# Optimization experiments

Hardware: AMD Instinct MI355X
Metric: run time of the kernel (lower is better)

The kernel has to match this reference:

```python
import jax, jax.numpy as jnp
import numpy as np

N = 30000   # nodes
E = 480000  # edges (avg degree 16)
D = 256     # feat_dim == dim
H = 8       # heads
C = 32      # out channels per head (D // H, concat=True)
NEG = 0.2   # leaky-relu negative slope (args.alpha)
L = 2       # num_layers
NENC = 2 * L  # two GATv2 encoders (source/target direction) per layer


def setup_inputs() -> dict:
    key = jax.random.key(0)
    ks = jax.random.split(key, 10)
    s = jax.random.normal(ks[0], (N, D), dtype=jnp.float32)
    t = jax.random.normal(ks[1], (N, D), dtype=jnp.float32)
    edge_index = jax.random.randint(ks[2], (2, E), 0, N, dtype=jnp.int32)
    scale = 0.05
    Wl = jax.random.normal(ks[3], (NENC, D, H * C), dtype=jnp.float32) * scale
    bl = jnp.zeros((NENC, H * C), dtype=jnp.float32)
    Wr = jax.random.normal(ks[4], (NENC, D, H * C), dtype=jnp.float32) * scale
    br = jnp.zeros((NENC, H * C), dtype=jnp.float32)
    att = jax.random.normal(ks[5], (NENC, H, C), dtype=jnp.float32) * scale
    bias = jnp.zeros((NENC, H * C), dtype=jnp.float32)
    return {"s": s, "t": t, "Wl": Wl, "bl": bl, "Wr": Wr, "br": br,
            "att": att, "bias": bias, "edge_index": edge_index}


def _gatv2(x_src, x_dst, src, dst, Wl, bl, Wr, br, att, bias):
    """PyG GATv2Conv on bipartite input ((x_src, x_dst), edge_index).
    Messages flow src->dst, softmax-normalized over incoming edges of dst."""
    hl = (x_src @ Wl + bl).reshape(N, H, C)  # lin_l(source)
    hr = (x_dst @ Wr + br).reshape(N, H, C)  # lin_r(target)
    xe = hl[src] + hr[dst]                    # [E,H,C]
    e = jnp.where(xe > 0, xe, NEG * xe)       # leaky_relu
    logits = jnp.einsum('ehc,hc->eh', e, att)  # [E,H]
    m = jax.ops.segment_max(logits, dst, num_segments=N)
    m = jnp.where(jnp.isfinite(m), m, jnp.zeros_like(m))  # empty segments
    p = jnp.exp(logits - m[dst])
    denom = jax.ops.segment_sum(p, dst, num_segments=N)
    alpha = p / (denom[dst] + 1e-16)          # scatter-softmax weights [E,H]
    out = jax.ops.segment_sum(alpha[:, :, None] * hl[src], dst, num_segments=N)
    return out.reshape(N, H * C) + bias       # concat heads + bias


def reference(s, t, Wl, bl, Wr, br, att, bias, edge_index):
    src, dst = edge_index[0], edge_index[1]
    x_s, x_t = s, t
    for l in range(L):
        i, j = 2 * l, 2 * l + 1
        # source_encoder((s, t), edges): aggregate s-messages at t-nodes
        sh = _gatv2(x_s, x_t, src, dst, Wl[i], bl[i], Wr[i], br[i], att[i], bias[i])
        # target_encoder((t, s), flipped edges)
        th = _gatv2(x_t, x_s, dst, src, Wl[j], bl[j], Wr[j], br[j], att[j], bias[j])
        if l < L - 1:  # last layer activation is identity
            sh = jax.nn.relu(sh)
            th = jax.nn.relu(th)
        x_s, x_t = sh, th
    return x_s, x_t
```

## Files before the change

### kernel.cpp

```cpp
#include <hip/hip_runtime.h>
#include <hip/hip_bf16.h>

#define NNODES 30000
#define NEDGES 480000
#define HC 256
#define NEG_SLOPE 0.2f
#define NPART 8
#define EPP 60000
#define PN (NPART * NNODES)
#define SCAN_CHUNK 1024
#define NCHUNK2 235
#define NCHUNKM 30
#define CPP 235
#define NFE 7680000

typedef _Float16 half8 __attribute__((ext_vector_type(8)));
typedef _Float16 h4v __attribute__((ext_vector_type(4)));
typedef _Float16 h2 __attribute__((ext_vector_type(2)));
typedef float floatx4 __attribute__((ext_vector_type(4)));


__global__ void prep_kernel(const float* __restrict__ Wl, const float* __restrict__ Wr,
                            _Float16* __restrict__ WtL, _Float16* __restrict__ WtR,
                            const int* __restrict__ ei, int* __restrict__ deg_dst,
                            int* __restrict__ deg_src) {
    __shared__ float sh[32][33];
    int b = blockIdx.x;
    if (b < 512) {
        int e = b >> 6;
        int r0 = ((b >> 3) & 7) * 32, c0 = (b & 7) * 32;
        const float* W = (e < 4) ? Wl + (size_t)e * 65536 : Wr + (size_t)(e - 4) * 65536;
        _Float16* Wt = (e < 4) ? WtL + (size_t)e * 65536 : WtR + (size_t)(e - 4) * 65536;
        int x = threadIdx.x & 31, y = threadIdx.x >> 5;
#pragma unroll
        for (int j = 0; j < 4; j++) {
            int r = y + j * 8;
            sh[r][x] = W[(size_t)(r0 + r) * 256 + c0 + x];
        }
        __syncthreads();
#pragma unroll
        for (int j = 0; j < 4; j++) {
            int nn = y + j * 8;
            Wt[(size_t)(c0 + nn) * 256 + r0 + x] = (_Float16)sh[x][nn];
        }
    } else {
        b -= 512;
        int p = b & 7, c = b >> 3;
        int idx = c * 256 + threadIdx.x;
        if (idx >= EPP) return;
        int e = p * EPP + idx;
        int s = ei[e];
        int d = ei[NEDGES + e];
        atomicAdd(&deg_dst[p * NNODES + d], 1);
        atomicAdd(&deg_src[p * NNODES + s], 1);
    }
}

__global__ void mdeg_kernel(const int* __restrict__ deg_dst, const int* __restrict__ deg_src,
                            int* __restrict__ mdeg_dst, int* __restrict__ mdeg_src) {
    const int* deg = blockIdx.y ? deg_src : deg_dst;
    int* mdeg = blockIdx.y ? mdeg_src : mdeg_dst;
    int n = blockIdx.x * blockDim.x + threadIdx.x;
    if (n >= NNODES) return;
    int s = 0;
#pragma unroll
    for (int p = 0; p < NPART; p++) s += deg[p * NNODES + n];
    mdeg[n] = s;
}


__global__ void scanA_kernel(const int* __restrict__ deg_dst, const int* __restrict__ deg_src,
                             const int* __restrict__ mdeg_dst, const int* __restrict__ mdeg_src,
                             int* __restrict__ cur_dst, int* __restrict__ cur_src,
                             int* __restrict__ mrp_dst, int* __restrict__ mrp_src,
                             int* __restrict__ bsum) {
    __shared__ int sh[SCAN_CHUNK];
    const int y = blockIdx.y;
    const int nelem = (y < 2) ? PN : NNODES;
    if (blockIdx.x * SCAN_CHUNK >= nelem) return;
    const int* in = (y == 0) ? deg_dst : (y == 1) ? deg_src : (y == 2) ? mdeg_dst : mdeg_src;
    int t = threadIdx.x;
    int gid = blockIdx.x * SCAN_CHUNK + t;
    int v = (gid < nelem) ? in[gid] : 0;
    sh[t] = v;
    __syncthreads();
    for (int off = 1; off < SCAN_CHUNK; off <<= 1) {
        int u = (t >= off) ? sh[t - off] : 0;
        __syncthreads();
        sh[t] += u;
        __syncthreads();
    }
    if (gid < nelem) {
        if (y < 2) {
            int* cur = (y == 0) ? cur_dst : cur_src;
            cur[gid] = sh[t] - v;
        } else {
            int* mrp = (y == 2) ? mrp_dst : mrp_src;
            mrp[gid + 1] = sh[t];
        }
    }
    if (t == SCAN_CHUNK - 1) bsum[y * 256 + blockIdx.x] = sh[t];
}

__global__ void scan2_kernel(int* __restrict__ bsum) {
    int t = threadIdx.x;
    if (t < 4) {
        int cnt = (t < 2) ? NCHUNK2 : NCHUNKM;
        int run = 0;
        for (int i = 0; i < cnt; i++) {
            int v = bsum[t * 256 + i];
            bsum[t * 256 + i] = run;
            run += v;
        }
    }
}

__global__ void scanB_kernel(int* __restrict__ cur_dst, int* __restrict__ cur_src,
                             int* __restrict__ mrp_dst, int* __restrict__ mrp_src,
                             const int* __restrict__ bsum) {
    const int y = blockIdx.y;
    const int nelem = (y < 2) ? PN : NNODES;
    if (blockIdx.x * SCAN_CHUNK >= nelem) return;
    int t = threadIdx.x;
    int gid = blockIdx.x * SCAN_CHUNK + t;
    int base = bsum[y * 256 + blockIdx.x];
    if (gid < nelem) {
        if (y < 2) {
            ((y == 0) ? cur_dst : cur_src)[gid] += base;
        } else {
            ((y == 2) ? mrp_dst : mrp_src)[gid + 1] += base;
        }
    }
    if (gid == 0 && y >= 2) ((y == 2) ? mrp_dst : mrp_src)[0] = 0;
}

__global__ void fill_kernel(const int* __restrict__ ei, int* __restrict__ cur_dst,
                            int* __restrict__ cur_src, unsigned short* __restrict__ col_dst,
                            unsigned short* __restrict__ col_src) {
    int p = blockIdx.x & 7, c = blockIdx.x >> 3;
    int idx = c * 256 + threadIdx.x;
    if (idx >= EPP) return;
    int e = p * EPP + idx;
    int s = ei[e];
    int d = ei[NEDGES + e];
    int p0 = atomicAdd(&cur_dst[p * NNODES + d], 1);
    col_dst[p0] = (unsigned short)s;
    int p1 = atomicAdd(&cur_src[p * NNODES + s], 1);
    col_src[p1] = (unsigned short)d;
}

__global__ void merge_kernel(const int* __restrict__ deg_dst, const int* __restrict__ deg_src,
                             const int* __restrict__ cur_dst, const int* __restrict__ cur_src,
                             const int* __restrict__ mrp_dst, const int* __restrict__ mrp_src,
                             const unsigned short* __restrict__ col_dst,
                             const unsigned short* __restrict__ col_src,
                             unsigned short* __restrict__ mcol_dst,
                             unsigned short* __restrict__ mcol_src) {
    const int z = blockIdx.y;
    const int* deg = z ? deg_src : deg_dst;
    const int* cur = z ? cur_src : cur_dst;
    const int* mrp = z ? mrp_src : mrp_dst;
    const unsigned short* col = z ? col_src : col_dst;
    unsigned short* mcol = z ? mcol_src : mcol_dst;
    int n = blockIdx.x * blockDim.x + threadIdx.x;
    if (n >= NNODES) return;
    int w = mrp[n];
#pragma unroll
    for (int p = 0; p < NPART; p++) {
        int e = cur[p * NNODES + n];
        int d = deg[p * NNODES + n];
        for (int k = e - d; k < e; k++) mcol[w++] = col[k];
    }
}


__device__ inline half8 ldA8(const _Float16* p) { return *(const half8*)p; }
__device__ inline half8 ldA8(const float* p) {
    float4 a = *(const float4*)p;
    float4 b = *(const float4*)(p + 4);
    half8 r = {(_Float16)a.x, (_Float16)a.y, (_Float16)a.z, (_Float16)a.w,
               (_Float16)b.x, (_Float16)b.y, (_Float16)b.z, (_Float16)b.w};
    return r;
}

#define EPI_STRIDE 264

template <typename AT>
__global__ void __launch_bounds__(256)
gemm_f16(const AT* __restrict__ xs, const AT* __restrict__ xt,
         const _Float16* __restrict__ WtL, const _Float16* __restrict__ WtR,
         const float* __restrict__ bl, const float* __restrict__ br,
         _Float16* __restrict__ hbase, int e0) {
    const int y = blockIdx.y;
    const int e = e0 + (y >> 1);
    const AT* A = (y == 0 || y == 3) ? xs : xt;
    const bool left = (y & 1) == 0;
    const _Float16* Wt = (left ? WtL : WtR) + (size_t)e * 65536;
    const float* bvec = (left ? bl : br) + (size_t)e * HC;
    _Float16* C = hbase + (size_t)y * NFE;

    __shared__ __align__(16) _Float16 sh[10240];
    _Float16* As = sh;
    _Float16* Bs = sh + 2048;

    const int t = threadIdx.x;
    const int lane = t & 63, w = t >> 6;
    const int m0 = blockIdx.x * 64;
    const int rl = lane & 15, ch = lane >> 4;
    const int ar = t >> 2, ac = t & 3;

    floatx4 acc[4][4] = {};

    half8 av = {};
    {
        int gr = m0 + ar;
        if (gr < NNODES) av = ldA8(A + (size_t)gr * 256 + ac * 8);
    }
    half8 bv[4];
#pragma unroll
    for (int j = 0; j < 4; j++)
        bv[j] = *(const half8*)(Wt + (size_t)(ar + j * 64) * 256 + ac * 8);

    for (int k0 = 0; k0 < 256; k0 += 32) {
        __syncthreads();
        *(half8*)(As + ar * 32 + (ac ^ ((ar >> 1) & 3)) * 8) = av;
#pragma unroll
        for (int j = 0; j < 4; j++) {
            int n = ar + j * 64;
            *(half8*)(Bs + n * 32 + (ac ^ ((n >> 1) & 3)) * 8) = bv[j];
        }
        __syncthreads();

        if (k0 + 32 < 256) {
            int gr = m0 + ar;
            if (gr < NNODES) av = ldA8(A + (size_t)gr * 256 + (k0 + 32) + ac * 8);
#pragma unroll
            for (int j = 0; j < 4; j++)
                bv[j] = *(const half8*)(Wt + (size_t)(ar + j * 64) * 256 + (k0 + 32) + ac * 8);
        }

        half8 a[4], b[4];
#pragma unroll
        for (int fm = 0; fm < 4; fm++) {
            int r = fm * 16 + rl;
            a[fm] = *(const half8*)(As + r * 32 + (ch ^ ((r >> 1) & 3)) * 8);
        }
#pragma unroll
        for (int fn = 0; fn < 4; fn++) {
            int n = w * 64 + fn * 16 + rl;
            b[fn] = *(const half8*)(Bs + n * 32 + (ch ^ ((n >> 1) & 3)) * 8);
        }
#pragma unroll
        for (int fm = 0; fm < 4; fm++)
#pragma unroll
            for (int fn = 0; fn < 4; fn++)
                acc[fm][fn] = __builtin_amdgcn_mfma_f32_16x16x32_f16(a[fm], b[fn], acc[fm][fn], 0, 0, 0);
    }

    float bb[4];
#pragma unroll
    for (int fn = 0; fn < 4; fn++) bb[fn] = bvec[w * 64 + fn * 16 + rl];

#pragma unroll
    for (int hh = 0; hh < 2; hh++) {
        __syncthreads();
#pragma unroll
        for (int f2 = 0; f2 < 2; f2++) {
            int fm = hh * 2 + f2;
#pragma unroll
            for (int fn = 0; fn < 4; fn++) {
                int colb = w * 64 + fn * 16 + rl;
#pragma unroll
                for (int j = 0; j < 4; j++) {
                    int lr = f2 * 16 + ch * 4 + j;
                    sh[lr * EPI_STRIDE + colb] = (_Float16)(acc[fm][fn][j] + bb[fn]);
                }
            }
        }
        __syncthreads();
        int lr = t >> 3;
        int cseg = (t & 7) * 32;
        int gr = m0 + hh * 32 + lr;
        if (gr < NNODES) {
#pragma unroll
            for (int q = 0; q < 4; q++)
                *(half8*)(C + (size_t)gr * 256 + cseg + q * 8) =
                    *(const half8*)(sh + lr * EPI_STRIDE + cseg + q * 8);
        }
    }
}


__device__ __forceinline__ void edge_body(half8 hv, half8 hrv, const float* att8,
                                          float* acc, float& denom, bool valid) {
    const h2 negv = {(_Float16)NEG_SLOPE, (_Float16)NEG_SLOPE};
    const h2* hvp = (const h2*)&hv;
    const h2* hrp = (const h2*)&hrv;
    float v = 0.f;
#pragma unroll
    for (int k = 0; k < 4; k++) {
        h2 x = hvp[k] + hrp[k];
        h2 lk = __builtin_elementwise_max(x, x * negv);
        v = fmaf((float)lk[0], att8[2 * k], v);
        v = fmaf((float)lk[1], att8[2 * k + 1], v);
    }
    v += __shfl_xor(v, 1);
    v += __shfl_xor(v, 2);
    float pe = __expf(v);
    if (!valid) pe = 0.f;
    denom += pe;
#pragma unroll
    for (int k = 0; k < 8; k++) acc[k] = fmaf((float)hv[k], pe, acc[k]);
}

__device__ inline void store8(float* p, const float* o) {
    *(float4*)p = make_float4(o[0], o[1], o[2], o[3]);
    *(float4*)(p + 4) = make_float4(o[4], o[5], o[6], o[7]);
}
__device__ inline void store8(_Float16* p, const float* o) {
    half8 h = {(_Float16)o[0], (_Float16)o[1], (_Float16)o[2], (_Float16)o[3],
               (_Float16)o[4], (_Float16)o[5], (_Float16)o[6], (_Float16)o[7]};
    *(half8*)p = h;
}

template <typename OT>
__global__ void __launch_bounds__(256)
agg_kernel(const _Float16* __restrict__ hbase,
           const int* __restrict__ mrp_dst, const unsigned short* __restrict__ mcol_dst,
           const int* __restrict__ mrp_src, const unsigned short* __restrict__ mcol_src,
           const float* __restrict__ att, const float* __restrict__ bias,
           OT* __restrict__ out0, OT* __restrict__ out1, int e0, int do_relu) {
    const int z = blockIdx.y;
    const _Float16* hl = hbase + (size_t)z * 2 * NFE;
    const _Float16* hr = hl + NFE;
    const int* mrp = z ? mrp_src : mrp_dst;
    const unsigned short* mcol = z ? mcol_src : mcol_dst;
    const float* attz = att + (size_t)(e0 + z) * HC;
    const float* biasz = bias + (size_t)(e0 + z) * HC;
    OT* out = z ? out1 : out0;

    int wave = threadIdx.x >> 6;
    int lane = threadIdx.x & 63;
    int n = blockIdx.x * 4 + wave;
    if (n >= NNODES) return;
    int h = lane >> 5;
    int cl = lane & 31;
    int c8 = cl << 3;

    const _Float16* hlc = hl + c8;
    half8 hrv = *(const half8*)(hr + (size_t)n * HC + c8);
    float att8[8];
    *(float4*)(att8) = *(const float4*)(attz + c8);
    *(float4*)(att8 + 4) = *(const float4*)(attz + c8 + 4);

    float acc[8] = {};
    float denom = 0.f;
    int beg = mrp[n], end = mrp[n + 1];

    int i = beg;
    for (; i + 8 <= end; i += 8) {
        int s0 = (int)mcol[i + h];
        int s1 = (int)mcol[i + 2 + h];
        int s2 = (int)mcol[i + 4 + h];
        int s3 = (int)mcol[i + 6 + h];
        half8 hv0 = *(const half8*)(hlc + ((size_t)s0 << 8));
        half8 hv1 = *(const half8*)(hlc + ((size_t)s1 << 8));
        half8 hv2 = *(const half8*)(hlc + ((size_t)s2 << 8));
        half8 hv3 = *(const half8*)(hlc + ((size_t)s3 << 8));
        edge_body(hv0, hrv, att8, acc, denom, true);
        edge_body(hv1, hrv, att8, acc, denom, true);
        edge_body(hv2, hrv, att8, acc, denom, true);
        edge_body(hv3, hrv, att8, acc, denom, true);
    }
    for (; i + 2 <= end; i += 2) {
        int s0 = (int)mcol[i + h];
        half8 hv0 = *(const half8*)(hlc + ((size_t)s0 << 8));
        edge_body(hv0, hrv, att8, acc, denom, true);
    }
    if (i < end) {
        bool valid = (h == 0);
        int s0 = (int)mcol[i];
        half8 hv0 = *(const half8*)(hlc + ((size_t)s0 << 8));
        edge_body(hv0, hrv, att8, acc, denom, valid);
    }

#pragma unroll
    for (int k = 0; k < 8; k++) acc[k] += __shfl_xor(acc[k], 32);
    denom += __shfl_xor(denom, 32);

    if (lane < 32) {
        float inv = 1.f / (denom + 1e-16f);
        float o[8];
        float b8[8];
        *(float4*)(b8) = *(const float4*)(biasz + c8);
        *(float4*)(b8 + 4) = *(const float4*)(biasz + c8 + 4);
#pragma unroll
        for (int k = 0; k < 8; k++) {
            o[k] = acc[k] * inv + b8[k];
            if (do_relu) o[k] = fmaxf(o[k], 0.f);
        }
        store8(out + (size_t)n * HC + c8, o);
    }
}


extern "C" void kernel_launch(void* const* d_in, const int* in_sizes, int n_in,
                              void* d_out, int out_size, void* d_ws, size_t ws_size,
                              hipStream_t stream) {
    const float* s = (const float*)d_in[0];
    const float* t = (const float*)d_in[1];
    const float* Wl = (const float*)d_in[2];
    const float* bl = (const float*)d_in[3];
    const float* Wr = (const float*)d_in[4];
    const float* br = (const float*)d_in[5];
    const float* att = (const float*)d_in[6];
    const float* bias = (const float*)d_in[7];
    const int* ei = (const int*)d_in[8];
    float* out = (float*)d_out;

    const size_t NF = (size_t)NFE;

    _Float16* os16 = (_Float16*)d_ws;
    _Float16* ot16 = os16 + NF;
    _Float16* hbase = ot16 + NF;
    _Float16* WtL = hbase + 4 * NF;
    _Float16* WtR = WtL + 4 * 65536;
    int* deg_dst = (int*)(WtR + 4 * 65536);
    int* deg_src = deg_dst + PN;
    int* cur_dst = deg_src + PN;
    int* cur_src = cur_dst + PN;
    int* mdeg_dst = cur_src + PN;
    int* mdeg_src = mdeg_dst + NNODES;
    int* mrp_dst = mdeg_src + NNODES;
    int* mrp_src = mrp_dst + (NNODES + 1);
    int* bsum = mrp_src + (NNODES + 1);
    unsigned short* col_dst = (unsigned short*)(bsum + 1024);
    unsigned short* col_src = col_dst + NEDGES;
    unsigned short* mcol_dst = col_src + NEDGES;
    unsigned short* mcol_src = mcol_dst + NEDGES;

    hipMemsetAsync(deg_dst, 0, 2 * PN * sizeof(int), stream);
    prep_kernel<<<512 + NPART * CPP, 256, 0, stream>>>(Wl, Wr, WtL, WtR, ei, deg_dst, deg_src);
    mdeg_kernel<<<dim3(118, 2), 256, 0, stream>>>(deg_dst, deg_src, mdeg_dst, mdeg_src);
    {
        dim3 g(NCHUNK2, 4);
        scanA_kernel<<<g, SCAN_CHUNK, 0, stream>>>(deg_dst, deg_src, mdeg_dst, mdeg_src,
                                                   cur_dst, cur_src, mrp_dst, mrp_src, bsum);
        scan2_kernel<<<1, 64, 0, stream>>>(bsum);
        scanB_kernel<<<g, SCAN_CHUNK, 0, stream>>>(cur_dst, cur_src, mrp_dst, mrp_src, bsum);
    }
    fill_kernel<<<NPART * CPP, 256, 0, stream>>>(ei, cur_dst, cur_src, col_dst, col_src);
    merge_kernel<<<dim3(118, 2), 256, 0, stream>>>(deg_dst, deg_src, cur_dst, cur_src,
                                                   mrp_dst, mrp_src, col_dst, col_src,
                                                   mcol_dst, mcol_src);

    dim3 ggemm((NNODES + 63) / 64, 4);
    dim3 gagg((NNODES + 3) / 4, 2);

    gemm_f16<float><<<ggemm, 256, 0, stream>>>(s, t, WtL, WtR, bl, br, hbase, 0);
    agg_kernel<_Float16><<<gagg, 256, 0, stream>>>(hbase, mrp_dst, mcol_dst, mrp_src, mcol_src,
                                                   att, bias, os16, ot16, 0, 1);
    gemm_f16<_Float16><<<ggemm, 256, 0, stream>>>(os16, ot16, WtL, WtR, bl, br, hbase, 2);
    agg_kernel<float><<<gagg, 256, 0, stream>>>(hbase, mrp_dst, mcol_dst, mrp_src, mcol_src,
                                                att, bias, out, out + NF, 2, 0);
}
```

Measured before the change: 377.6 us.

## Split aggregation per head with 8-edge parallel waves and fuse degree merge into scan

The aggregation kernel now assigns one wave per (node, head) pair, with 8 lanes covering the head's 32 channels (4 each) and 8 edges processed in parallel per iteration. Attention logits use packed fp16 dot products, and partial sums are reduced across the edge groups at the end. The separate mdeg kernel is removed; the scan kernel sums the per-partition degrees directly. This aims to raise occupancy and parallelism per node and to cut one launch, at the cost of 8x more blocks and more shuffle reductions, plus fp16 dot precision for the logits.

Measured after the change: 648.8 us. 1.72x slower.

```diff
diff --git a/kernel.cpp b/kernel.cpp
--- a/kernel.cpp
+++ b/kernel.cpp
@@ -56,21 +56,8 @@
     }
 }
 
-__global__ void mdeg_kernel(const int* __restrict__ deg_dst, const int* __restrict__ deg_src,
-                            int* __restrict__ mdeg_dst, int* __restrict__ mdeg_src) {
-    const int* deg = blockIdx.y ? deg_src : deg_dst;
-    int* mdeg = blockIdx.y ? mdeg_src : mdeg_dst;
-    int n = blockIdx.x * blockDim.x + threadIdx.x;
-    if (n >= NNODES) return;
-    int s = 0;
-#pragma unroll
-    for (int p = 0; p < NPART; p++) s += deg[p * NNODES + n];
-    mdeg[n] = s;
-}
-
 
 __global__ void scanA_kernel(const int* __restrict__ deg_dst, const int* __restrict__ deg_src,
-                             const int* __restrict__ mdeg_dst, const int* __restrict__ mdeg_src,
                              int* __restrict__ cur_dst, int* __restrict__ cur_src,
                              int* __restrict__ mrp_dst, int* __restrict__ mrp_src,
                              int* __restrict__ bsum) {
@@ -78,10 +65,18 @@
     const int y = blockIdx.y;
     const int nelem = (y < 2) ? PN : NNODES;
     if (blockIdx.x * SCAN_CHUNK >= nelem) return;
-    const int* in = (y == 0) ? deg_dst : (y == 1) ? deg_src : (y == 2) ? mdeg_dst : mdeg_src;
     int t = threadIdx.x;
     int gid = blockIdx.x * SCAN_CHUNK + t;
-    int v = (gid < nelem) ? in[gid] : 0;
+    int v = 0;
+    if (gid < nelem) {
+        if (y == 0) v = deg_dst[gid];
+        else if (y == 1) v = deg_src[gid];
+        else {
+            const int* deg = (y == 2) ? deg_dst : deg_src;
+#pragma unroll
+            for (int p = 0; p < NPART; p++) v += deg[p * NNODES + gid];
+        }
+    }
     sh[t] = v;
     __syncthreads();
     for (int off = 1; off < SCAN_CHUNK; off <<= 1) {
@@ -92,11 +87,9 @@
     }
     if (gid < nelem) {
         if (y < 2) {
-            int* cur = (y == 0) ? cur_dst : cur_src;
-            cur[gid] = sh[t] - v;
+            ((y == 0) ? cur_dst : cur_src)[gid] = sh[t] - v;
         } else {
-            int* mrp = (y == 2) ? mrp_dst : mrp_src;
-            mrp[gid + 1] = sh[t];
+            ((y == 2) ? mrp_dst : mrp_src)[gid + 1] = sh[t];
         }
     }
     if (t == SCAN_CHUNK - 1) bsum[y * 256 + blockIdx.x] = sh[t];
@@ -291,36 +284,13 @@
 }
 
 
-__device__ __forceinline__ void edge_body(half8 hv, half8 hrv, const float* att8,
-                                          float* acc, float& denom, bool valid) {
-    const h2 negv = {(_Float16)NEG_SLOPE, (_Float16)NEG_SLOPE};
-    const h2* hvp = (const h2*)&hv;
-    const h2* hrp = (const h2*)&hrv;
-    float v = 0.f;
-#pragma unroll
-    for (int k = 0; k < 4; k++) {
-        h2 x = hvp[k] + hrp[k];
-        h2 lk = __builtin_elementwise_max(x, x * negv);
-        v = fmaf((float)lk[0], att8[2 * k], v);
-        v = fmaf((float)lk[1], att8[2 * k + 1], v);
-    }
-    v += __shfl_xor(v, 1);
-    v += __shfl_xor(v, 2);
-    float pe = __expf(v);
-    if (!valid) pe = 0.f;
-    denom += pe;
-#pragma unroll
-    for (int k = 0; k < 8; k++) acc[k] = fmaf((float)hv[k], pe, acc[k]);
-}
-
-__device__ inline void store8(float* p, const float* o) {
-    *(float4*)p = make_float4(o[0], o[1], o[2], o[3]);
-    *(float4*)(p + 4) = make_float4(o[4], o[5], o[6], o[7]);
-}
-__device__ inline void store8(_Float16* p, const float* o) {
-    half8 h = {(_Float16)o[0], (_Float16)o[1], (_Float16)o[2], (_Float16)o[3],
-               (_Float16)o[4], (_Float16)o[5], (_Float16)o[6], (_Float16)o[7]};
-    *(half8*)p = h;
+__device__ inline void stslice(float* p, float o0, float o1, float o2, float o3) {
+    floatx4 v = {o0, o1, o2, o3};
+    *(floatx4*)p = v;
+}
+__device__ inline void stslice(_Float16* p, float o0, float o1, float o2, float o3) {
+    h4v h = {(_Float16)o0, (_Float16)o1, (_Float16)o2, (_Float16)o3};
+    *(h4v*)p = h;
 }
 
 template <typename OT>
@@ -339,67 +309,73 @@
     const float* biasz = bias + (size_t)(e0 + z) * HC;
     OT* out = z ? out1 : out0;
 
-    int wave = threadIdx.x >> 6;
-    int lane = threadIdx.x & 63;
-    int n = blockIdx.x * 4 + wave;
+    const int wave = threadIdx.x >> 6;
+    const int lane = threadIdx.x & 63;
+    const int head = blockIdx.x & 7;
+    const int n = (blockIdx.x >> 3) * 4 + wave;
     if (n >= NNODES) return;
-    int h = lane >> 5;
-    int cl = lane & 31;
-    int c8 = cl << 3;
-
-    const _Float16* hlc = hl + c8;
-    half8 hrv = *(const half8*)(hr + (size_t)n * HC + c8);
-    float att8[8];
-    *(float4*)(att8) = *(const float4*)(attz + c8);
-    *(float4*)(att8 + 4) = *(const float4*)(attz + c8 + 4);
-
-    float acc[8] = {};
-    float denom = 0.f;
+    const int g = lane >> 3;
+    const int cl = lane & 7;
+    const int c = (head << 5) + (cl << 2);
+
+    const _Float16* hlc = hl + c;
+    h4v hrv = *(const h4v*)(hr + (size_t)n * HC + c);
+    float4 a4 = *(const float4*)(attz + c);
+    const h2 at0 = {(_Float16)a4.x, (_Float16)a4.y};
+    const h2 at1 = {(_Float16)a4.z, (_Float16)a4.w};
+    const h2 negv = {(_Float16)NEG_SLOPE, (_Float16)NEG_SLOPE};
+    const h2 hr0 = {hrv[0], hrv[1]};
+    const h2 hr1 = {hrv[2], hrv[3]};
+
+    float acc0 = 0.f, acc1 = 0.f, acc2 = 0.f, acc3 = 0.f, denom = 0.f;
     int beg = mrp[n], end = mrp[n + 1];
 
-    int i = beg;
-    for (; i + 8 <= end; i += 8) {
-        int s0 = (int)mcol[i + h];
-        int s1 = (int)mcol[i + 2 + h];
-        int s2 = (int)mcol[i + 4 + h];
-        int s3 = (int)mcol[i + 6 + h];
-        half8 hv0 = *(const half8*)(hlc + ((size_t)s0 << 8));
-        half8 hv1 = *(const half8*)(hlc + ((size_t)s1 << 8));
-        half8 hv2 = *(const half8*)(hlc + ((size_t)s2 << 8));
-        half8 hv3 = *(const half8*)(hlc + ((size_t)s3 << 8));
-        edge_body(hv0, hrv, att8, acc, denom, true);
-        edge_body(hv1, hrv, att8, acc, denom, true);
-        edge_body(hv2, hrv, att8, acc, denom, true);
-        edge_body(hv3, hrv, att8, acc, denom, true);
-    }
-    for (; i + 2 <= end; i += 2) {
-        int s0 = (int)mcol[i + h];
-        half8 hv0 = *(const half8*)(hlc + ((size_t)s0 << 8));
-        edge_body(hv0, hrv, att8, acc, denom, true);
-    }
-    if (i < end) {
-        bool valid = (h == 0);
-        int s0 = (int)mcol[i];
-        half8 hv0 = *(const half8*)(hlc + ((size_t)s0 << 8));
-        edge_body(hv0, hrv, att8, acc, denom, valid);
-    }
-
-#pragma unroll
-    for (int k = 0; k < 8; k++) acc[k] += __shfl_xor(acc[k], 32);
-    denom += __shfl_xor(denom, 32);
-
-    if (lane < 32) {
+    for (int i = beg; i < end; i += 8) {
+        int eid = i + g;
+        bool valid = eid < end;
+        int s = (int)mcol[valid ? eid : i];
+        h4v hv = *(const h4v*)(hlc + ((size_t)s << 8));
+        h2 x0 = h2{hv[0], hv[1]} + hr0;
+        h2 x1 = h2{hv[2], hv[3]} + hr1;
+        h2 l0 = __builtin_elementwise_max(x0, x0 * negv);
+        h2 l1 = __builtin_elementwise_max(x1, x1 * negv);
+        float v = __builtin_amdgcn_fdot2(l0, at0, 0.f, false);
+        v = __builtin_amdgcn_fdot2(l1, at1, v, false);
+        v += __shfl_xor(v, 1);
+        v += __shfl_xor(v, 2);
+        v += __shfl_xor(v, 4);
+        float pe = __expf(v);
+        if (!valid) pe = 0.f;
+        denom += pe;
+        acc0 = fmaf((float)hv[0], pe, acc0);
+        acc1 = fmaf((float)hv[1], pe, acc1);
+        acc2 = fmaf((float)hv[2], pe, acc2);
+        acc3 = fmaf((float)hv[3], pe, acc3);
+    }
+
+#pragma unroll
+    for (int off = 8; off < 64; off <<= 1) {
+        denom += __shfl_xor(denom, off);
+        acc0 += __shfl_xor(acc0, off);
+        acc1 += __shfl_xor(acc1, off);
+        acc2 += __shfl_xor(acc2, off);
+        acc3 += __shfl_xor(acc3, off);
+    }
+
+    if (lane < 8) {
         float inv = 1.f / (denom + 1e-16f);
-        float o[8];
-        float b8[8];
-        *(float4*)(b8) = *(const float4*)(biasz + c8);
-        *(float4*)(b8 + 4) = *(const float4*)(biasz + c8 + 4);
-#pragma unroll
-        for (int k = 0; k < 8; k++) {
-            o[k] = acc[k] * inv + b8[k];
-            if (do_relu) o[k] = fmaxf(o[k], 0.f);
-        }
-        store8(out + (size_t)n * HC + c8, o);
+        float4 b4 = *(const float4*)(biasz + c);
+        float o0 = acc0 * inv + b4.x;
+        float o1 = acc1 * inv + b4.y;
+        float o2 = acc2 * inv + b4.z;
+        float o3 = acc3 * inv + b4.w;
+        if (do_relu) {
+            o0 = fmaxf(o0, 0.f);
+            o1 = fmaxf(o1, 0.f);
+            o2 = fmaxf(o2, 0.f);
+            o3 = fmaxf(o3, 0.f);
+        }
+        stslice(out + (size_t)n * HC + c, o0, o1, o2, o3);
     }
 }
 
@@ -429,9 +405,7 @@
     int* deg_src = deg_dst + PN;
     int* cur_dst = deg_src + PN;
     int* cur_src = cur_dst + PN;
-    int* mdeg_dst = cur_src + PN;
-    int* mdeg_src = mdeg_dst + NNODES;
-    int* mrp_dst = mdeg_src + NNODES;
+    int* mrp_dst = cur_src + PN;
     int* mrp_src = mrp_dst + (NNODES + 1);
     int* bsum = mrp_src + (NNODES + 1);
     unsigned short* col_dst = (unsigned short*)(bsum + 1024);
@@ -441,11 +415,10 @@
 
     hipMemsetAsync(deg_dst, 0, 2 * PN * sizeof(int), stream);
     prep_kernel<<<512 + NPART * CPP, 256, 0, stream>>>(Wl, Wr, WtL, WtR, ei, deg_dst, deg_src);
-    mdeg_kernel<<<dim3(118, 2), 256, 0, stream>>>(deg_dst, deg_src, mdeg_dst, mdeg_src);
     {
         dim3 g(NCHUNK2, 4);
-        scanA_kernel<<<g, SCAN_CHUNK, 0, stream>>>(deg_dst, deg_src, mdeg_dst, mdeg_src,
-                                                   cur_dst, cur_src, mrp_dst, mrp_src, bsum);
+        scanA_kernel<<<g, SCAN_CHUNK, 0, stream>>>(deg_dst, deg_src, cur_dst, cur_src,
+                                                   mrp_dst, mrp_src, bsum);
         scan2_kernel<<<1, 64, 0, stream>>>(bsum);
         scanB_kernel<<<g, SCAN_CHUNK, 0, stream>>>(cur_dst, cur_src, mrp_dst, mrp_src, bsum);
     }
@@ -455,7 +428,7 @@
                                                    mcol_dst, mcol_src);
 
     dim3 ggemm((NNODES + 63) / 64, 4);
-    dim3 gagg((NNODES + 3) / 4, 2);
+    dim3 gagg(((NNODES + 3) / 4) * 8, 2);
 
     gemm_f16<float><<<ggemm, 256, 0, stream>>>(s, t, WtL, WtR, bl, br, hbase, 0);
     agg_kernel<_Float16><<<gagg, 256, 0, stream>>>(hbase, mrp_dst, mcol_dst, mrp_src, mcol_src,
```
